# Performance work log

Measured on AMD Instinct MI355X. Metric: run time of the kernel, lower is better.

The kernel has to match this reference:

```python
import jax, jax.numpy as jnp
import numpy as np

N, F, P, O, E = 20000, 8, 12, 32, 320000


def setup_inputs() -> dict:
    key = jax.random.key(0)
    ks = jax.random.split(key, 18)
    g = lambda k, shape: (jax.random.normal(k, shape, jnp.float32) * 0.1)
    x = jax.random.normal(ks[0], (N, F, P), jnp.float32)
    edge_index = jax.random.randint(ks[1], (2, E), 0, N, dtype=jnp.int32)
    return {
        "x": x,
        "edge_index": edge_index,
        # GCNConv weights/biases for update (z), reset (r), candidate (h) gates
        "Wz": g(ks[2], (F, O)), "bz": g(ks[3], (O,)),
        "Wr": g(ks[4], (F, O)), "br": g(ks[5], (O,)),
        "Wh": g(ks[6], (F, O)), "bh": g(ks[7], (O,)),
        # GRU linear layers (torch.nn.Linear: y = x @ W.T + b), in=2*O, out=O
        "lz_w": g(ks[8], (O, 2 * O)), "lz_b": g(ks[9], (O,)),
        "lr_w": g(ks[10], (O, 2 * O)), "lr_b": g(ks[11], (O,)),
        "lh_w": g(ks[12], (O, 2 * O)), "lh_b": g(ks[13], (O,)),
        # temporal attention logits over periods
        "att": g(ks[14], (P,)),
        # final Linear(32 -> window_size)
        "out_w": g(ks[15], (P, O)), "out_b": g(ks[16], (P,)),
    }


def reference(x, edge_index, Wz, bz, Wr, br, Wh, bh,
              lz_w, lz_b, lr_w, lr_b, lh_w, lh_b, att, out_w, out_b):
    n = x.shape[0]
    # gcn_norm with self-loops: norm_e = d^-1/2[src] * d^-1/2[dst]
    loop = jnp.arange(n, dtype=edge_index.dtype)
    src = jnp.concatenate([edge_index[0], loop])
    dst = jnp.concatenate([edge_index[1], loop])
    deg = jax.ops.segment_sum(jnp.ones(src.shape[0], x.dtype), dst, num_segments=n)
    dinv = jnp.where(deg > 0, deg ** -0.5, 0.0)
    norm = dinv[src] * dinv[dst]  # [E+n]

    def gcn(xp, W, b):
        # xp: [n, P, F] -> [n, P, O]; GCNConv: D^-1/2 (A+I) D^-1/2 (X W) + b
        h = jnp.einsum('npf,fo->npo', xp, W)
        msg = h[src] * norm[:, None, None]  # [E+n, P, O]
        return jax.ops.segment_sum(msg, dst, num_segments=n) + b

    xp = jnp.transpose(x, (0, 2, 1))  # [n, P, F]
    # A3TGCN does NOT carry H across periods (H stays initial zeros), so all
    # periods are independent GRU steps from H = 0 and can be batched.
    H = jnp.zeros(xp.shape[:2] + (O,), x.dtype)
    Z = jax.nn.sigmoid(jnp.concatenate([gcn(xp, Wz, bz), H], -1) @ lz_w.T + lz_b)
    R = jax.nn.sigmoid(jnp.concatenate([gcn(xp, Wr, br), H], -1) @ lr_w.T + lr_b)
    Ht = jnp.tanh(jnp.concatenate([gcn(xp, Wh, bh), H * R], -1) @ lh_w.T + lh_b)
    Hp = Z * H + (1.0 - Z) * Ht  # [n, P, O]
    probs = jax.nn.softmax(att)
    Hacc = jnp.einsum('npo,p->no', Hp, probs)  # attention-weighted sum
    return jax.nn.relu(Hacc) @ out_w.T + out_b  # [n, window_size]
```

## Files before the change

kernel.cpp:

```cpp
#include <hip/hip_runtime.h>
#include <math.h>

#define FP 96
#define SLOT 64
#define NPB 8
#define GBLK 128
#define PBLK 256
#define POISON ((int)0xAAAAAAAA)

__device__ __forceinline__ unsigned f2bf_bits(float f) {
    unsigned u = __float_as_uint(f);
    return (u + 0x7fffu + ((u >> 16) & 1u)) >> 16;
}
__device__ __forceinline__ float bf_lo(unsigned u) { return __uint_as_float(u << 16); }
__device__ __forceinline__ float bf_hi(unsigned u) { return __uint_as_float(u & 0xffff0000u); }

__device__ __forceinline__ int cnt_decode(int v) {
    return ((unsigned)v >= 0xAA000000u) ? v - POISON : v;
}

__global__ void k_hist_fold(const int* __restrict__ ei, int E,
                            int* __restrict__ cnt, int* __restrict__ bucket,
                            const float* __restrict__ Wz, const float* __restrict__ bz,
                            const float* __restrict__ Wh, const float* __restrict__ bh,
                            const float* __restrict__ lz_w, const float* __restrict__ lz_b,
                            const float* __restrict__ lh_w, const float* __restrict__ lh_b,
                            const float* __restrict__ att, const float* __restrict__ out_w,
                            const float* __restrict__ out_b, float* __restrict__ cst) {
    int b = blockIdx.x, t = threadIdx.x;
    if (b == gridDim.x - 1) {
        int f = t >> 5, o = t & 31;
        float sz = 0.f, sh = 0.f;
        for (int j = 0; j < 32; ++j) {
            sz += Wz[f * 32 + j] * lz_w[o * 64 + j];
            sh += Wh[f * 32 + j] * lh_w[o * 64 + j];
        }
        cst[t]       = sz;
        cst[256 + t] = sh;
        if (t < 32) {
            float a = lz_b[t], c = lh_b[t];
            for (int j = 0; j < 32; ++j) {
                a += bz[j] * lz_w[t * 64 + j];
                c += bh[j] * lh_w[t * 64 + j];
            }
            cst[512 + t] = a;
            cst[544 + t] = c;
        }
        if (t < 12) {
            float m = -1e30f;
            for (int p = 0; p < 12; ++p) m = fmaxf(m, att[p]);
            float s = 0.f;
            for (int p = 0; p < 12; ++p) s += expf(att[p] - m);
            cst[576 + t] = expf(att[t] - m) / s;
        }
        for (int i = t; i < 384; i += PBLK)
            cst[588 + (i & 31) * 12 + (i >> 5)] = out_w[i];
        if (t < 12) cst[972 + t] = out_b[t];
        return;
    }
    int e = b * PBLK + t;
    if (e >= E) return;
    int src = ei[e], dst = ei[E + e];
    int old = atomicAdd(cnt + dst, 1);
    int pos = cnt_decode(old);
    if (pos < SLOT) bucket[(size_t)dst * SLOT + pos] = src;
}

__global__ void k_convert(const float* __restrict__ x, const int* __restrict__ cnt,
                          unsigned* __restrict__ xb, int N) {
    int i = blockIdx.x * blockDim.x + threadIdx.x;
    if (i >= (N + 1) * 12) return;
    int n = i / 12;
    if (n == N) {
        ((uint4*)xb)[i] = make_uint4(0u, 0u, 0u, 0u);
        return;
    }
    int deg = cnt_decode(cnt[n]);
    float w = rsqrtf((float)(deg + 1));
    const float4* x4 = (const float4*)x;
    float4 a = x4[i * 2], c = x4[i * 2 + 1];
    uint4 r;
    r.x = f2bf_bits(w * a.x) | (f2bf_bits(w * a.y) << 16);
    r.y = f2bf_bits(w * a.z) | (f2bf_bits(w * a.w) << 16);
    r.z = f2bf_bits(w * c.x) | (f2bf_bits(w * c.y) << 16);
    r.w = f2bf_bits(w * c.z) | (f2bf_bits(w * c.w) << 16);
    ((uint4*)xb)[i] = r;
}

__device__ __forceinline__ void load_batch(uint4* P, const uint4* __restrict__ xrow,
                                           const int* list, int k) {
#pragma unroll
    for (int u = 0; u < 8; ++u) P[u] = xrow[list[u] * 12 + k];
}
__device__ __forceinline__ void acc_batch(float* acc, const uint4* C) {
    acc[0] += ((bf_lo(C[0].x) + bf_lo(C[1].x)) + (bf_lo(C[2].x) + bf_lo(C[3].x)))
            + ((bf_lo(C[4].x) + bf_lo(C[5].x)) + (bf_lo(C[6].x) + bf_lo(C[7].x)));
    acc[1] += ((bf_hi(C[0].x) + bf_hi(C[1].x)) + (bf_hi(C[2].x) + bf_hi(C[3].x)))
            + ((bf_hi(C[4].x) + bf_hi(C[5].x)) + (bf_hi(C[6].x) + bf_hi(C[7].x)));
    acc[2] += ((bf_lo(C[0].y) + bf_lo(C[1].y)) + (bf_lo(C[2].y) + bf_lo(C[3].y)))
            + ((bf_lo(C[4].y) + bf_lo(C[5].y)) + (bf_lo(C[6].y) + bf_lo(C[7].y)));
    acc[3] += ((bf_hi(C[0].y) + bf_hi(C[1].y)) + (bf_hi(C[2].y) + bf_hi(C[3].y)))
            + ((bf_hi(C[4].y) + bf_hi(C[5].y)) + (bf_hi(C[6].y) + bf_hi(C[7].y)));
    acc[4] += ((bf_lo(C[0].z) + bf_lo(C[1].z)) + (bf_lo(C[2].z) + bf_lo(C[3].z)))
            + ((bf_lo(C[4].z) + bf_lo(C[5].z)) + (bf_lo(C[6].z) + bf_lo(C[7].z)));
    acc[5] += ((bf_hi(C[0].z) + bf_hi(C[1].z)) + (bf_hi(C[2].z) + bf_hi(C[3].z)))
            + ((bf_hi(C[4].z) + bf_hi(C[5].z)) + (bf_hi(C[6].z) + bf_hi(C[7].z)));
    acc[6] += ((bf_lo(C[0].w) + bf_lo(C[1].w)) + (bf_lo(C[2].w) + bf_lo(C[3].w)))
            + ((bf_lo(C[4].w) + bf_lo(C[5].w)) + (bf_lo(C[6].w) + bf_lo(C[7].w)));
    acc[7] += ((bf_hi(C[0].w) + bf_hi(C[1].w)) + (bf_hi(C[2].w) + bf_hi(C[3].w)))
            + ((bf_hi(C[4].w) + bf_hi(C[5].w)) + (bf_hi(C[6].w) + bf_hi(C[7].w)));
}

__global__ void __launch_bounds__(GBLK)
k_gather_gates(const unsigned* __restrict__ xb, const int* __restrict__ cnt,
               const int* __restrict__ bucket, const float* __restrict__ cst,
               float* __restrict__ out, int N) {
    __shared__ float sy[NPB][FP + 4];
    __shared__ float shr[NPB][32];
    __shared__ float scst[984];
    __shared__ int   sbuck[NPB][72];
    __shared__ int   sdeg[NPB];
    int t = threadIdx.x;
    int n0 = blockIdx.x * NPB;
    const uint4* xrow = (const uint4*)xb;

    int nl = 0, k = 0, n = N;
    uint4 self = make_uint4(0u, 0u, 0u, 0u);
    if (t < NPB * 12) {
        nl = t / 12; k = t - nl * 12; n = n0 + nl;
        if (n < N) self = xrow[n * 12 + k];
    }
    if (t < NPB) sdeg[t] = (n0 + t < N) ? cnt_decode(cnt[n0 + t]) : 0;
    {
        int nd = t >> 4, q = t & 15, nn = n0 + nd;
        if (nn < N) *(int4*)&sbuck[nd][q * 4] =
            ((const int4*)(bucket + (size_t)nn * SLOT))[q];
    }
    for (int i = t; i < 984; i += GBLK) scst[i] = cst[i];
    __syncthreads();
    if (t < NPB * 8) {
        int nnl = t >> 3, q = t & 7;
        int d = min(sdeg[nnl], SLOT);
        int degp = (d + 7) & ~7; if (degp < 8) degp = 8;
        int pos = d + q;
        if (pos < degp) sbuck[nnl][pos] = N;
    }
    __syncthreads();

    if (t < NPB * 12 && n < N) {
        int c = sdeg[nl];
        int d = min(c, SLOT);
        int degp = (d + 7) & ~7; if (degp < 8) degp = 8;
        int nb = degp >> 3;
        int nA = (nb + 1) >> 1;
        int nB = nb - nA;
        const int* list = sbuck[nl];
        float acc[8] = {bf_lo(self.x), bf_hi(self.x), bf_lo(self.y), bf_hi(self.y),
                        bf_lo(self.z), bf_hi(self.z), bf_lo(self.w), bf_hi(self.w)};
        uint4 A[8], B[8];
        load_batch(A, xrow, list, k);
        if (nB > 0) load_batch(B, xrow, list + nA * 8, k);
        for (int i = 0; i < nA; ++i) {
            uint4 CA[8];
#pragma unroll
            for (int u = 0; u < 8; ++u) CA[u] = A[u];
            if (i + 1 < nA) load_batch(A, xrow, list + (i + 1) * 8, k);
            acc_batch(acc, CA);
            if (i < nB) {
                uint4 CB[8];
#pragma unroll
                for (int u = 0; u < 8; ++u) CB[u] = B[u];
                if (i + 1 < nB) load_batch(B, xrow, list + (nA + i + 1) * 8, k);
                acc_batch(acc, CB);
            }
        }
        float di = rsqrtf((float)(c + 1));
#pragma unroll
        for (int i = 0; i < 8; ++i) sy[nl][k * 8 + i] = di * acc[i];
    }
    __syncthreads();

    int o = t & 31;
#pragma unroll
    for (int it = 0; it < 2; ++it) {
        int local = (t >> 5) + it * 4, nn = n0 + local;
        if (nn < N) {
            float cz = scst[512 + o], ch = scst[544 + o];
            float hacc = 0.f;
#pragma unroll
            for (int p = 0; p < 12; ++p) {
                float az = cz, ah = ch;
#pragma unroll
                for (int f = 0; f < 8; ++f) {
                    float xf = sy[local][f * 12 + p];
                    az += xf * scst[f * 32 + o];
                    ah += xf * scst[256 + f * 32 + o];
                }
                float Z  = 1.f / (1.f + expf(-az));
                float Ht = tanhf(ah);
                hacc += scst[576 + p] * (1.f - Z) * Ht;
            }
            shr[local][o] = fmaxf(hacc, 0.f);
        }
    }
    __syncthreads();
#pragma unroll
    for (int it = 0; it < 2; ++it) {
        int local = (t >> 5) + it * 4, nn = n0 + local;
        if (nn < N && o < 12) {
            float s = scst[972 + o];
#pragma unroll
            for (int j2 = 0; j2 < 32; ++j2)
                s += shr[local][j2] * scst[588 + j2 * 12 + o];
            out[(size_t)nn * 12 + o] = s;
        }
    }
}

extern "C" void kernel_launch(void* const* d_in, const int* in_sizes, int n_in,
                              void* d_out, int out_size, void* d_ws, size_t ws_size,
                              hipStream_t stream) {
    const float* x    = (const float*)d_in[0];
    const int*   ei   = (const int*)d_in[1];
    const float* Wz   = (const float*)d_in[2];
    const float* bz   = (const float*)d_in[3];
    const float* Wh   = (const float*)d_in[6];
    const float* bh   = (const float*)d_in[7];
    const float* lz_w = (const float*)d_in[8];
    const float* lz_b = (const float*)d_in[9];
    const float* lh_w = (const float*)d_in[12];
    const float* lh_b = (const float*)d_in[13];
    const float* att  = (const float*)d_in[14];
    const float* ow   = (const float*)d_in[15];
    const float* ob   = (const float*)d_in[16];
    float* out = (float*)d_out;

    int N = in_sizes[0] / FP;
    int E = in_sizes[1] / 2;

    int*      cnt    = (int*)d_ws;
    int*      bucket = cnt + (N + 1);
    unsigned* xb     = (unsigned*)(bucket + (size_t)N * SLOT);
    float*    cst    = (float*)(xb + (size_t)(N + 1) * 48);

    int EB = (E + PBLK - 1) / PBLK;
    k_hist_fold<<<EB + 1, PBLK, 0, stream>>>(ei, E, cnt, bucket, Wz, bz, Wh, bh,
                                             lz_w, lz_b, lh_w, lh_b, att, ow, ob, cst);
    k_convert  <<<((N + 1) * 12 + PBLK - 1) / PBLK, PBLK, 0, stream>>>(x, cnt, xb, N);
    k_gather_gates<<<(N + NPB - 1) / NPB, GBLK, 0, stream>>>(xb, cnt, bucket, cst, out, N);
}
```

Before: 143.0 us.

## Vectorize edge bucketing, simplify gather pipeline, use fast sigmoid/tanh intrinsics

Each histogram thread now handles two edges with int2 loads, halving the block count. The gather loop drops the dual A/B prefetch streams for a single double-buffered stream, and launch bounds now request 4 blocks per CU to lower register pressure. Sigmoid and tanh use __expf and hardware reciprocal approximations instead of expf/tanhf. The cost is less memory-level parallelism in the gather and slightly lower accuracy in the gate activations.

```diff
diff --git a/kernel.cpp b/kernel.cpp
--- a/kernel.cpp
+++ b/kernel.cpp
@@ -58,12 +58,23 @@
         if (t < 12) cst[972 + t] = out_b[t];
         return;
     }
-    int e = b * PBLK + t;
+    int e2 = b * PBLK + t;
+    int e = e2 << 1;
     if (e >= E) return;
-    int src = ei[e], dst = ei[E + e];
-    int old = atomicAdd(cnt + dst, 1);
-    int pos = cnt_decode(old);
-    if (pos < SLOT) bucket[(size_t)dst * SLOT + pos] = src;
+    if (e + 1 < E) {
+        int2 s2 = ((const int2*)ei)[e2];
+        int2 d2 = ((const int2*)(ei + E))[e2];
+        int o0 = atomicAdd(cnt + d2.x, 1);
+        int o1 = atomicAdd(cnt + d2.y, 1);
+        int p0 = cnt_decode(o0), p1 = cnt_decode(o1);
+        if (p0 < SLOT) bucket[(size_t)d2.x * SLOT + p0] = s2.x;
+        if (p1 < SLOT) bucket[(size_t)d2.y * SLOT + p1] = s2.y;
+    } else {
+        int src = ei[e], dst = ei[E + e];
+        int old = atomicAdd(cnt + dst, 1);
+        int pos = cnt_decode(old);
+        if (pos < SLOT) bucket[(size_t)dst * SLOT + pos] = src;
+    }
 }
 
 __global__ void k_convert(const float* __restrict__ x, const int* __restrict__ cnt,
@@ -111,7 +122,7 @@
             + ((bf_hi(C[4].w) + bf_hi(C[5].w)) + (bf_hi(C[6].w) + bf_hi(C[7].w)));
 }
 
-__global__ void __launch_bounds__(GBLK)
+__global__ void __launch_bounds__(GBLK, 4)
 k_gather_gates(const unsigned* __restrict__ xb, const int* __restrict__ cnt,
                const int* __restrict__ bucket, const float* __restrict__ cst,
                float* __restrict__ out, int N) {
@@ -152,27 +163,16 @@
         int d = min(c, SLOT);
         int degp = (d + 7) & ~7; if (degp < 8) degp = 8;
         int nb = degp >> 3;
-        int nA = (nb + 1) >> 1;
-        int nB = nb - nA;
         const int* list = sbuck[nl];
         float acc[8] = {bf_lo(self.x), bf_hi(self.x), bf_lo(self.y), bf_hi(self.y),
                         bf_lo(self.z), bf_hi(self.z), bf_lo(self.w), bf_hi(self.w)};
-        uint4 A[8], B[8];
+        uint4 A[8], C[8];
         load_batch(A, xrow, list, k);
-        if (nB > 0) load_batch(B, xrow, list + nA * 8, k);
-        for (int i = 0; i < nA; ++i) {
-            uint4 CA[8];
-#pragma unroll
-            for (int u = 0; u < 8; ++u) CA[u] = A[u];
-            if (i + 1 < nA) load_batch(A, xrow, list + (i + 1) * 8, k);
-            acc_batch(acc, CA);
-            if (i < nB) {
-                uint4 CB[8];
-#pragma unroll
-                for (int u = 0; u < 8; ++u) CB[u] = B[u];
-                if (i + 1 < nB) load_batch(B, xrow, list + (nA + i + 1) * 8, k);
-                acc_batch(acc, CB);
-            }
+        for (int i = 0; i < nb; ++i) {
+#pragma unroll
+            for (int u = 0; u < 8; ++u) C[u] = A[u];
+            if (i + 1 < nb) load_batch(A, xrow, list + (i + 1) * 8, k);
+            acc_batch(acc, C);
         }
         float di = rsqrtf((float)(c + 1));
 #pragma unroll
@@ -196,8 +196,10 @@
                     az += xf * scst[f * 32 + o];
                     ah += xf * scst[256 + f * 32 + o];
                 }
-                float Z  = 1.f / (1.f + expf(-az));
-                float Ht = tanhf(ah);
+                float ez = __expf(-az);
+                float Z  = __builtin_amdgcn_rcpf(1.f + ez);
+                float eh = __expf(ah + ah);
+                float Ht = 1.f - 2.f * __builtin_amdgcn_rcpf(eh + 1.f);
                 hacc += scst[576 + p] * (1.f - Z) * Ht;
             }
             shr[local][o] = fmaxf(hacc, 0.f);
@@ -243,7 +245,7 @@
     unsigned* xb     = (unsigned*)(bucket + (size_t)N * SLOT);
     float*    cst    = (float*)(xb + (size_t)(N + 1) * 48);
 
-    int EB = (E + PBLK - 1) / PBLK;
+    int EB = (E + PBLK * 2 - 1) / (PBLK * 2);
     k_hist_fold<<<EB + 1, PBLK, 0, stream>>>(ei, E, cnt, bucket, Wz, bz, Wh, bh,
                                              lz_w, lz_b, lh_w, lh_b, att, ow, ob, cst);
     k_convert  <<<((N + 1) * 12 + PBLK - 1) / PBLK, PBLK, 0, stream>>>(x, cnt, xb, N);
```

Result: faster. 131.2 us (-8.3%).
